# Kernel optimization log

Hardware: AMD Instinct MI355X
Metric: run time of the kernel (lower is better)

Reference implementation:

```python
import jax, jax.numpy as jnp
import numpy as np
from jax import lax

DIM = 128
EXP = 4
K = 7
B, D, H, W = 2, 48, 48, 48


def setup_inputs() -> dict:
    key = jax.random.key(0)
    ks = jax.random.split(key, 8)
    C, Ch = DIM, EXP * DIM
    x = jax.random.normal(ks[0], (B, C, D, H, W), dtype=jnp.float32)
    dw_w = jax.random.normal(ks[1], (C, 1, K, K, K), dtype=jnp.float32) * 0.05
    dw_b = jnp.zeros((C,), dtype=jnp.float32)
    ln_g = jnp.ones((C,), dtype=jnp.float32)
    ln_b = jnp.zeros((C,), dtype=jnp.float32)
    w1 = jax.random.normal(ks[2], (C, Ch), dtype=jnp.float32) * (1.0 / np.sqrt(C))
    b1 = jnp.zeros((Ch,), dtype=jnp.float32)
    grn_g = jnp.zeros((Ch,), dtype=jnp.float32)
    grn_b = jnp.zeros((Ch,), dtype=jnp.float32)
    w2 = jax.random.normal(ks[3], (Ch, C), dtype=jnp.float32) * (1.0 / np.sqrt(Ch))
    b2 = jnp.zeros((C,), dtype=jnp.float32)
    return {"x": x, "dw_w": dw_w, "dw_b": dw_b, "ln_g": ln_g, "ln_b": ln_b,
            "w1": w1, "b1": b1, "grn_g": grn_g, "grn_b": grn_b, "w2": w2, "b2": b2}


def reference(x, dw_w, dw_b, ln_g, ln_b, w1, b1, grn_g, grn_b, w2, b2):
    C = x.shape[1]
    pad = (K - 1) // 2
    # depthwise 3D conv, NCDHW
    y = lax.conv_general_dilated(
        x, dw_w, window_strides=(1, 1, 1),
        padding=[(pad, pad)] * 3,
        feature_group_count=C,
        dimension_numbers=("NCDHW", "OIDHW", "NCDHW"))
    y = y + dw_b[None, :, None, None, None]
    y = jnp.transpose(y, (0, 2, 3, 4, 1))  # [B,D,H,W,C] channels-last
    # LayerNorm over channels (eps=1e-6)
    mu = jnp.mean(y, axis=-1, keepdims=True)
    var = jnp.mean((y - mu) ** 2, axis=-1, keepdims=True)
    y = (y - mu) / jnp.sqrt(var + 1e-6) * ln_g + ln_b
    # pwconv1 + GELU (exact)
    h = jax.nn.gelu(jnp.einsum("bdhwc,ce->bdhwe", y, w1) + b1, approximate=False)
    # GRN: global L2 over spatial dims per channel, divisive norm over channel mean
    gx = jnp.sqrt(jnp.sum(h * h, axis=(1, 2, 3), keepdims=True))  # [B,1,1,1,Ch]
    nx = gx / (jnp.mean(gx, axis=-1, keepdims=True) + 1e-6)
    h = grn_g * (h * nx) + grn_b + h
    # pwconv2
    y = jnp.einsum("bdhwe,ec->bdhwc", h, w2) + b2
    y = jnp.transpose(y, (0, 4, 1, 2, 3))  # back to NCDHW
    return x + y
```

## Files before the change

### kernel.cpp

```cpp
#include <hip/hip_runtime.h>
#include <math.h>

#define PVOX 110592
#define CDIM 128
#define EDIM 512

typedef __attribute__((ext_vector_type(8))) short short8_t;
typedef __attribute__((ext_vector_type(4))) float float4_t;

__device__ __forceinline__ unsigned short f2bf(float f) {
  unsigned int u = __float_as_uint(f);
  unsigned int r = (u + 0x7FFFu + ((u >> 16) & 1u)) >> 16;
  return (unsigned short)r;
}
__device__ __forceinline__ float bf2f(unsigned short s) {
  return __uint_as_float(((unsigned int)s) << 16);
}
__device__ __forceinline__ int swz(int row, int col) {
  return (row << 7) + ((((col >> 3) ^ (row & 15)) << 3) | (col & 7));
}
__device__ __forceinline__ int swzO(int c, int p) {
  return (c << 7) + (p ^ ((c & 15) << 2));
}

__global__ __launch_bounds__(256) void k0_wprep(
    const float* __restrict__ w1, const float* __restrict__ w2,
    unsigned short* __restrict__ w1t, unsigned short* __restrict__ w2t) {
  int idx = blockIdx.x * 256 + threadIdx.x;
  int e = idx >> 7, c = idx & 127;
  w1t[e * 128 + c] = f2bf(w1[c * 512 + e]);
  w2t[c * 512 + e] = f2bf(w2[e * 128 + c]);
}

__global__ __launch_bounds__(576, 4) void k1_dwconv(
    const float* __restrict__ x, const float* __restrict__ dw_w,
    const float* __restrict__ dw_b, float* __restrict__ yconv) {
  __shared__ float sx[2][54 * 60];
  int bx = blockIdx.x;
  int dh = bx & 1;
  int c = (bx >> 1) & 127;
  int b = bx >> 8;
  int d0 = dh * 24;
  const float* xp = x + (size_t)(b * 128 + c) * PVOX;
  float* yp = yconv + (size_t)(b * 128 + c) * PVOX;
  const float* wbase = dw_w + c * 343;
  float bias = dw_b[c];
  int t = threadIdx.x;
  int h = t / 12, wc = t % 12;
  int w0 = wc * 4;
  for (int i = t; i < 2 * 54 * 60; i += 576) ((float*)sx)[i] = 0.f;
  __syncthreads();
  {
    int p = d0 - 3;
    if (p >= 0) {
      float4_t v = *(const float4_t*)&xp[((size_t)p * 48 + h) * 48 + w0];
      *(float4_t*)&sx[0][(h + 3) * 60 + 4 + w0] = v;
    }
  }
  float acc[7][4];
#pragma unroll
  for (int j = 0; j < 7; j++)
#pragma unroll
    for (int i = 0; i < 4; i++) acc[j][i] = bias;
  __syncthreads();

  for (int q = 0; q < 30; ++q) {
    int p = d0 - 3 + q;
    int pn = p + 1;
    bool ldok = (pn >= 0) && (pn <= 47) && (pn <= d0 + 26);
    float4_t stg = {0.f, 0.f, 0.f, 0.f};
    if (ldok) stg = *(const float4_t*)&xp[((size_t)pn * 48 + h) * 48 + w0];

    const float* bufr = sx[q & 1];
    if (p >= 0 && p <= 47) {
#pragma unroll
      for (int kh = 0; kh < 7; kh++) {
        const float* rp = &bufr[(h + kh) * 60 + w0];
        float4_t v0 = *(const float4_t*)&rp[0];
        float4_t v1 = *(const float4_t*)&rp[4];
        float4_t v2 = *(const float4_t*)&rp[8];
        float v[12] = {v0[0], v0[1], v0[2], v0[3], v1[0], v1[1], v1[2], v1[3],
                       v2[0], v2[1], v2[2], v2[3]};
#pragma unroll
        for (int kd = 0; kd < 7; kd++) {
          if ((unsigned)(q - kd) < 24u) {
            const float* wr = wbase + kd * 49 + kh * 7;
#pragma unroll
            for (int kw = 0; kw < 7; kw++) {
              float wv = wr[kw];
#pragma unroll
              for (int wi = 0; wi < 4; wi++)
                acc[6 - kd][wi] += wv * v[wi + kw + 1];
            }
          }
        }
      }
    }
    if (q >= 6) {
      int d = d0 + q - 6;
      float4_t o;
      o[0] = acc[0][0]; o[1] = acc[0][1]; o[2] = acc[0][2]; o[3] = acc[0][3];
      *(float4_t*)&yp[((size_t)d * 48 + h) * 48 + w0] = o;
    }
#pragma unroll
    for (int j = 0; j < 6; j++)
#pragma unroll
      for (int i = 0; i < 4; i++) acc[j][i] = acc[j + 1][i];
#pragma unroll
    for (int i = 0; i < 4; i++) acc[6][i] = bias;
    float* bufw = (float*)sx[(q + 1) & 1];
    *(float4_t*)&bufw[(h + 3) * 60 + 4 + w0] = stg;
    __syncthreads();
  }
}

__global__ __launch_bounds__(256) void k2_ln(
    const float* __restrict__ yconv, const float* __restrict__ ln_g,
    const float* __restrict__ ln_b, unsigned short* __restrict__ ycl) {
  __shared__ float sy[128 * 65];
  __shared__ float smean[64], srstd[64];
  int bx = blockIdx.x;
  int b = bx / 1728;
  int p0 = (bx % 1728) * 64;
  int t = threadIdx.x;
  int v = t & 63, c4 = t >> 6;
  const float* yp = yconv + (size_t)b * 128 * PVOX + p0;
  for (int cc = 0; cc < 32; cc++) {
    int c = cc * 4 + c4;
    sy[c * 65 + v] = yp[(size_t)c * PVOX + v];
  }
  __syncthreads();
  if (t < 64) {
    float s = 0.f, ss = 0.f;
    for (int c = 0; c < 128; c++) { float val = sy[c * 65 + t]; s += val; ss += val * val; }
    float mu = s * (1.f / 128.f);
    float var = ss * (1.f / 128.f) - mu * mu;
    smean[t] = mu; srstd[t] = rsqrtf(var + 1e-6f);
  }
  __syncthreads();
  unsigned short* op = ycl + ((size_t)b * PVOX + p0) * 128;
  for (int it = 0; it < 32; it++) {
    int idx = it * 256 + t;
    int vv = idx >> 7, c = idx & 127;
    float val = (sy[c * 65 + vv] - smean[vv]) * srstd[vv] * ln_g[c] + ln_b[c];
    op[vv * 128 + c] = f2bf(val);
  }
}

__global__ __launch_bounds__(256) void k3_pw1(
    const unsigned short* __restrict__ ycl, const unsigned short* __restrict__ w1t,
    const float* __restrict__ b1, unsigned short* __restrict__ h,
    float* __restrict__ gsum) {
  __shared__ short smem[2 * 128 * 128];
  short* sA = smem;
  short* sB = smem + 128 * 128;
  int bx = blockIdx.x;
  int et = bx & 3; int pt = bx >> 2;
  int e0 = et << 7;
  int b = (pt >= 864) ? 1 : 0;
  int t = threadIdx.x;
  for (int it = 0; it < 8; it++) {
    int flat = it * 2048 + t * 8;
    int row = flat >> 7, col = flat & 127;
    *(uint4*)&sA[swz(row, col)] = *(const uint4*)&ycl[((size_t)(pt * 128 + row)) * 128 + col];
    *(uint4*)&sB[swz(row, col)] = *(const uint4*)&w1t[(e0 + row) * 128 + col];
  }
  __syncthreads();
  int wave = t >> 6, lane = t & 63;
  int wm = (wave >> 1) * 64, wn = (wave & 1) * 64;
  int ln15 = lane & 15, q = lane >> 4;
  float4_t acc[4][4] = {};
  for (int kk = 0; kk < 4; kk++) {
    int k0 = kk * 32 + q * 8;
    short8_t af[4], bf[4];
#pragma unroll
    for (int i = 0; i < 4; i++)
      af[i] = *(const short8_t*)&sA[swz(wm + i * 16 + ln15, k0)];
#pragma unroll
    for (int j = 0; j < 4; j++)
      bf[j] = *(const short8_t*)&sB[swz(wn + j * 16 + ln15, k0)];
#pragma unroll
    for (int i = 0; i < 4; i++)
#pragma unroll
      for (int j = 0; j < 4; j++)
        acc[i][j] = __builtin_amdgcn_mfma_f32_16x16x32_bf16(af[i], bf[j], acc[i][j], 0, 0, 0);
  }
  __syncthreads();
  float biasv[4];
#pragma unroll
  for (int j = 0; j < 4; j++) biasv[j] = b1[e0 + wn + j * 16 + ln15];
  float ssq[4] = {0.f, 0.f, 0.f, 0.f};
#pragma unroll
  for (int i = 0; i < 4; i++) {
#pragma unroll
    for (int j = 0; j < 4; j++) {
      int e_local = wn + j * 16 + ln15;
#pragma unroll
      for (int r = 0; r < 4; r++) {
        float val = acc[i][j][r] + biasv[j];
        float g = 0.5f * val * (1.0f + erff(val * 0.70710678118f));
        ssq[j] += g * g;
        sA[swz(wm + i * 16 + q * 4 + r, e_local)] = (short)f2bf(g);
      }
    }
  }
#pragma unroll
  for (int j = 0; j < 4; j++) {
    ssq[j] += __shfl_xor(ssq[j], 16);
    ssq[j] += __shfl_xor(ssq[j], 32);
  }
  if (q == 0) {
#pragma unroll
    for (int j = 0; j < 4; j++)
      atomicAdd(&gsum[b * 512 + e0 + wn + j * 16 + ln15], ssq[j]);
  }
  __syncthreads();
  for (int it = 0; it < 8; it++) {
    int flat = it * 2048 + t * 8;
    int row = flat >> 7, col = flat & 127;
    *(uint4*)&h[((size_t)(pt * 128 + row)) * 512 + e0 + col] = *(const uint4*)&sA[swz(row, col)];
  }
}

__global__ __launch_bounds__(512) void k4_grn(
    const float* __restrict__ gsum, const float* __restrict__ grn_g,
    const float* __restrict__ grn_b, const float* __restrict__ w2,
    const float* __restrict__ b2, float* __restrict__ s, float* __restrict__ badd) {
  __shared__ float red[512];
  int t = threadIdx.x;
  for (int b = 0; b < 2; b++) {
    float gx = sqrtf(gsum[b * 512 + t]);
    red[t] = gx;
    __syncthreads();
    for (int off = 256; off > 0; off >>= 1) {
      if (t < off) red[t] += red[t + off];
      __syncthreads();
    }
    float mean = red[0] * (1.f / 512.f);
    __syncthreads();
    s[b * 512 + t] = 1.0f + grn_g[t] * (gx / (mean + 1e-6f));
  }
  if (t < 128) {
    float acc = b2[t];
    for (int e = 0; e < 512; e++) acc += grn_b[e] * w2[e * 128 + t];
    badd[t] = acc;
  }
}

__global__ __launch_bounds__(256) void k5_pw2(
    const unsigned short* __restrict__ h, const unsigned short* __restrict__ w2t,
    const float* __restrict__ s, const float* __restrict__ badd,
    const float* __restrict__ x, float* __restrict__ out) {
  __shared__ short smem[2 * 128 * 128];
  short* sA = smem;
  short* sB = smem + 128 * 128;
  int bx = blockIdx.x;
  int b = bx / 864;
  int p0 = (bx % 864) * 128;
  int vp0 = bx * 128;
  int t = threadIdx.x;
  int wave = t >> 6, lane = t & 63;
  int wm = (wave >> 1) * 64, wn = (wave & 1) * 64;
  int ln15 = lane & 15, q = lane >> 4;
  const float* sb = s + b * 512;
  float4_t acc[4][4] = {};
  for (int ec = 0; ec < 4; ec++) {
    int e0 = ec * 128;
    for (int it = 0; it < 8; it++) {
      int flat = it * 2048 + t * 8;
      int row = flat >> 7, col = flat & 127;
      uint4 raw = *(const uint4*)&h[((size_t)(vp0 + row)) * 512 + e0 + col];
      const unsigned short* us = (const unsigned short*)&raw;
      unsigned short ov[8];
#pragma unroll
      for (int i2 = 0; i2 < 8; i2++)
        ov[i2] = f2bf(bf2f(us[i2]) * sb[e0 + col + i2]);
      *(uint4*)&sA[swz(row, col)] = *(const uint4*)ov;
      *(uint4*)&sB[swz(row, col)] = *(const uint4*)&w2t[row * 512 + e0 + col];
    }
    __syncthreads();
    for (int kk = 0; kk < 4; kk++) {
      int k0 = kk * 32 + q * 8;
      short8_t af[4], bf[4];
#pragma unroll
      for (int i = 0; i < 4; i++)
        af[i] = *(const short8_t*)&sA[swz(wm + i * 16 + ln15, k0)];
#pragma unroll
      for (int j = 0; j < 4; j++)
        bf[j] = *(const short8_t*)&sB[swz(wn + j * 16 + ln15, k0)];
#pragma unroll
      for (int i = 0; i < 4; i++)
#pragma unroll
        for (int j = 0; j < 4; j++)
          acc[i][j] = __builtin_amdgcn_mfma_f32_16x16x32_bf16(af[i], bf[j], acc[i][j], 0, 0, 0);
    }
    __syncthreads();
  }
  float* sO = (float*)smem;
#pragma unroll
  for (int i = 0; i < 4; i++)
#pragma unroll
    for (int j = 0; j < 4; j++) {
      int c = wn + j * 16 + ln15;
#pragma unroll
      for (int r = 0; r < 4; r++)
        sO[swzO(c, wm + i * 16 + q * 4 + r)] = acc[i][j][r];
    }
  __syncthreads();
  for (int it = 0; it < 16; it++) {
    int flat4 = it * 256 + t;
    int c = flat4 >> 5, col4 = (flat4 & 31) * 4;
    float4_t v = *(const float4_t*)&sO[swzO(c, col4)];
    float bd = badd[c];
    size_t gi = (size_t)(b * 128 + c) * PVOX + p0 + col4;
    float4_t xv = *(const float4_t*)&x[gi];
    v[0] += bd + xv[0]; v[1] += bd + xv[1]; v[2] += bd + xv[2]; v[3] += bd + xv[3];
    *(float4_t*)&out[gi] = v;
  }
}

extern "C" void kernel_launch(void* const* d_in, const int* in_sizes, int n_in,
                              void* d_out, int out_size, void* d_ws, size_t ws_size,
                              hipStream_t stream) {
  (void)in_sizes; (void)n_in; (void)out_size; (void)ws_size;
  const float* x    = (const float*)d_in[0];
  const float* dw_w = (const float*)d_in[1];
  const float* dw_b = (const float*)d_in[2];
  const float* ln_g = (const float*)d_in[3];
  const float* ln_b = (const float*)d_in[4];
  const float* w1   = (const float*)d_in[5];
  const float* b1   = (const float*)d_in[6];
  const float* grn_g= (const float*)d_in[7];
  const float* grn_b= (const float*)d_in[8];
  const float* w2   = (const float*)d_in[9];
  const float* b2   = (const float*)d_in[10];
  float* outp = (float*)d_out;

  char* w = (char*)d_ws;
  float*          yconv = (float*)(w);
  unsigned short* ycl   = (unsigned short*)(w + 113246208);
  unsigned short* h     = (unsigned short*)(w + 169869312);
  float*          gsum  = (float*)(w + 396361728);
  float*          s     = (float*)(w + 396365824);
  float*          badd  = (float*)(w + 396369920);
  unsigned short* w1t   = (unsigned short*)(w + 396370432);
  unsigned short* w2t   = (unsigned short*)(w + 396501504);

  hipMemsetAsync(gsum, 0, 2 * 512 * sizeof(float), stream);
  k0_wprep<<<256, 256, 0, stream>>>(w1, w2, w1t, w2t);
  k1_dwconv<<<512, 576, 0, stream>>>(x, dw_w, dw_b, yconv);
  k2_ln<<<3456, 256, 0, stream>>>(yconv, ln_g, ln_b, ycl);
  k3_pw1<<<6912, 256, 0, stream>>>(ycl, w1t, b1, h, gsum);
  k4_grn<<<1, 512, 0, stream>>>(gsum, grn_g, grn_b, w2, b2, s, badd);
  k5_pw2<<<1728, 256, 0, stream>>>(h, w2t, s, badd, x, outp);
}
```

Before: 996.1 us.

## Retile depthwise conv into H/D tiles and loop pw1 over E tiles per block

```diff
diff --git a/kernel.cpp b/kernel.cpp
--- a/kernel.cpp
+++ b/kernel.cpp
@@ -32,29 +32,70 @@
   w2t[c * 512 + e] = f2bf(w2[e * 128 + c]);
 }
 
-__global__ __launch_bounds__(576, 4) void k1_dwconv(
+template <bool GUARD>
+__device__ __forceinline__ void conv_plane12(
+    const float* __restrict__ bufr, const float* __restrict__ wbase,
+    float (&acc)[7][4], int hl, int w0, int q) {
+#pragma unroll
+  for (int kh = 0; kh < 7; kh++) {
+    const float* rp = &bufr[(hl + kh) * 60 + w0];
+    float4_t v0 = *(const float4_t*)&rp[0];
+    float4_t v1 = *(const float4_t*)&rp[4];
+    float4_t v2 = *(const float4_t*)&rp[8];
+    float v[12] = {v0[0], v0[1], v0[2], v0[3], v1[0], v1[1], v1[2], v1[3],
+                   v2[0], v2[1], v2[2], v2[3]};
+#pragma unroll
+    for (int kd = 0; kd < 7; kd++) {
+      if (!GUARD || (unsigned)(q - kd) < 12u) {
+        const float* wr = wbase + kd * 49 + kh * 7;
+#pragma unroll
+        for (int kw = 0; kw < 7; kw++) {
+          float wv = wr[kw];
+#pragma unroll
+          for (int wi = 0; wi < 4; wi++)
+            acc[6 - kd][wi] += wv * v[wi + kw + 1];
+        }
+      }
+    }
+  }
+}
+
+__global__ __launch_bounds__(192) void k1_dwconv(
     const float* __restrict__ x, const float* __restrict__ dw_w,
     const float* __restrict__ dw_b, float* __restrict__ yconv) {
-  __shared__ float sx[2][54 * 60];
+  __shared__ float sx[2][22 * 60];
   int bx = blockIdx.x;
-  int dh = bx & 1;
-  int c = (bx >> 1) & 127;
-  int b = bx >> 8;
-  int d0 = dh * 24;
+  int h3 = bx % 3;
+  int dt4 = (bx / 3) & 3;
+  int c = (bx / 12) & 127;
+  int b = bx / 1536;
+  int dt0 = dt4 * 12, h0 = h3 * 16;
   const float* xp = x + (size_t)(b * 128 + c) * PVOX;
   float* yp = yconv + (size_t)(b * 128 + c) * PVOX;
   const float* wbase = dw_w + c * 343;
   float bias = dw_b[c];
   int t = threadIdx.x;
-  int h = t / 12, wc = t % 12;
-  int w0 = wc * 4;
-  for (int i = t; i < 2 * 54 * 60; i += 576) ((float*)sx)[i] = 0.f;
+  int hl = t / 12, wq = t % 12;
+  int w0 = wq * 4;
+  for (int i = t; i < 2 * 22 * 60; i += 192) ((float*)sx)[i] = 0.f;
   __syncthreads();
   {
-    int p = d0 - 3;
+    int p = dt0 - 3;
     if (p >= 0) {
-      float4_t v = *(const float4_t*)&xp[((size_t)p * 48 + h) * 48 + w0];
-      *(float4_t*)&sx[0][(h + 3) * 60 + 4 + w0] = v;
+      {
+        int gh = h0 - 3 + hl;
+        float4_t v = {0.f, 0.f, 0.f, 0.f};
+        if ((unsigned)gh < 48u)
+          v = *(const float4_t*)&xp[((size_t)p * 48 + gh) * 48 + wq * 4];
+        *(float4_t*)&sx[0][hl * 60 + 4 + wq * 4] = v;
+      }
+      if (t < 72) {
+        int gh = h0 + 13 + hl;
+        float4_t v = {0.f, 0.f, 0.f, 0.f};
+        if ((unsigned)gh < 48u)
+          v = *(const float4_t*)&xp[((size_t)p * 48 + gh) * 48 + wq * 4];
+        *(float4_t*)&sx[0][(hl + 16) * 60 + 4 + wq * 4] = v;
+      }
     }
   }
   float acc[7][4];
@@ -64,43 +105,54 @@
     for (int i = 0; i < 4; i++) acc[j][i] = bias;
   __syncthreads();
 
-  for (int q = 0; q < 30; ++q) {
-    int p = d0 - 3 + q;
-    int pn = p + 1;
-    bool ldok = (pn >= 0) && (pn <= 47) && (pn <= d0 + 26);
-    float4_t stg = {0.f, 0.f, 0.f, 0.f};
-    if (ldok) stg = *(const float4_t*)&xp[((size_t)pn * 48 + h) * 48 + w0];
-
-    const float* bufr = sx[q & 1];
-    if (p >= 0 && p <= 47) {
-#pragma unroll
-      for (int kh = 0; kh < 7; kh++) {
-        const float* rp = &bufr[(h + kh) * 60 + w0];
-        float4_t v0 = *(const float4_t*)&rp[0];
-        float4_t v1 = *(const float4_t*)&rp[4];
-        float4_t v2 = *(const float4_t*)&rp[8];
-        float v[12] = {v0[0], v0[1], v0[2], v0[3], v1[0], v1[1], v1[2], v1[3],
-                       v2[0], v2[1], v2[2], v2[3]};
-#pragma unroll
-        for (int kd = 0; kd < 7; kd++) {
-          if ((unsigned)(q - kd) < 24u) {
-            const float* wr = wbase + kd * 49 + kh * 7;
-#pragma unroll
-            for (int kw = 0; kw < 7; kw++) {
-              float wv = wr[kw];
-#pragma unroll
-              for (int wi = 0; wi < 4; wi++)
-                acc[6 - kd][wi] += wv * v[wi + kw + 1];
-            }
-          }
-        }
-      }
-    }
-    if (q >= 6) {
-      int d = d0 + q - 6;
+  for (int q = 0; q < 6; ++q) {
+    int p = dt0 - 3 + q, pn = p + 1;
+    bool ok = (pn >= 0);
+    float4_t sA = {0.f, 0.f, 0.f, 0.f}, sB = {0.f, 0.f, 0.f, 0.f};
+    if (ok) {
+      int gh = h0 - 3 + hl;
+      if ((unsigned)gh < 48u)
+        sA = *(const float4_t*)&xp[((size_t)pn * 48 + gh) * 48 + wq * 4];
+      if (t < 72) {
+        int gh2 = h0 + 13 + hl;
+        if ((unsigned)gh2 < 48u)
+          sB = *(const float4_t*)&xp[((size_t)pn * 48 + gh2) * 48 + wq * 4];
+      }
+    }
+    if (p >= 0)
+      conv_plane12<true>(sx[q & 1], wbase, acc, hl, w0, q);
+#pragma unroll
+    for (int j = 0; j < 6; j++)
+#pragma unroll
+      for (int i = 0; i < 4; i++) acc[j][i] = acc[j + 1][i];
+#pragma unroll
+    for (int i = 0; i < 4; i++) acc[6][i] = bias;
+    float* bw = (float*)sx[(q + 1) & 1];
+    *(float4_t*)&bw[hl * 60 + 4 + wq * 4] = sA;
+    if (t < 72) *(float4_t*)&bw[(hl + 16) * 60 + 4 + wq * 4] = sB;
+    __syncthreads();
+  }
+  for (int q = 6; q < 12; ++q) {
+    int pn = dt0 - 2 + q;
+    float4_t sA, sB = {0.f, 0.f, 0.f, 0.f};
+    {
+      int gh = h0 - 3 + hl;
+      float4_t v = {0.f, 0.f, 0.f, 0.f};
+      if ((unsigned)gh < 48u)
+        v = *(const float4_t*)&xp[((size_t)pn * 48 + gh) * 48 + wq * 4];
+      sA = v;
+      if (t < 72) {
+        int gh2 = h0 + 13 + hl;
+        if ((unsigned)gh2 < 48u)
+          sB = *(const float4_t*)&xp[((size_t)pn * 48 + gh2) * 48 + wq * 4];
+      }
+    }
+    conv_plane12<false>(sx[q & 1], wbase, acc, hl, w0, q);
+    {
+      int d = dt0 + q - 6;
       float4_t o;
       o[0] = acc[0][0]; o[1] = acc[0][1]; o[2] = acc[0][2]; o[3] = acc[0][3];
-      *(float4_t*)&yp[((size_t)d * 48 + h) * 48 + w0] = o;
+      *(float4_t*)&yp[((size_t)d * 48 + (h0 + hl)) * 48 + w0] = o;
     }
 #pragma unroll
     for (int j = 0; j < 6; j++)
@@ -108,8 +160,42 @@
       for (int i = 0; i < 4; i++) acc[j][i] = acc[j + 1][i];
 #pragma unroll
     for (int i = 0; i < 4; i++) acc[6][i] = bias;
-    float* bufw = (float*)sx[(q + 1) & 1];
-    *(float4_t*)&bufw[(h + 3) * 60 + 4 + w0] = stg;
+    float* bw = (float*)sx[(q + 1) & 1];
+    *(float4_t*)&bw[hl * 60 + 4 + wq * 4] = sA;
+    if (t < 72) *(float4_t*)&bw[(hl + 16) * 60 + 4 + wq * 4] = sB;
+    __syncthreads();
+  }
+  for (int q = 12; q < 18; ++q) {
+    int p = dt0 - 3 + q, pn = p + 1;
+    bool ok = (pn <= 47) && (pn <= dt0 + 14);
+    float4_t sA = {0.f, 0.f, 0.f, 0.f}, sB = {0.f, 0.f, 0.f, 0.f};
+    if (ok) {
+      int gh = h0 - 3 + hl;
+      if ((unsigned)gh < 48u)
+        sA = *(const float4_t*)&xp[((size_t)pn * 48 + gh) * 48 + wq * 4];
+      if (t < 72) {
+        int gh2 = h0 + 13 + hl;
+        if ((unsigned)gh2 < 48u)
+          sB = *(const float4_t*)&xp[((size_t)pn * 48 + gh2) * 48 + wq * 4];
+      }
+    }
+    if (p <= 47)
+      conv_plane12<true>(sx[q & 1], wbase, acc, hl, w0, q);
+    {
+      int d = dt0 + q - 6;
+      float4_t o;
+      o[0] = acc[0][0]; o[1] = acc[0][1]; o[2] = acc[0][2]; o[3] = acc[0][3];
+      *(float4_t*)&yp[((size_t)d * 48 + (h0 + hl)) * 48 + w0] = o;
+    }
+#pragma unroll
+    for (int j = 0; j < 6; j++)
+#pragma unroll
+      for (int i = 0; i < 4; i++) acc[j][i] = acc[j + 1][i];
+#pragma unroll
+    for (int i = 0; i < 4; i++) acc[6][i] = bias;
+    float* bw = (float*)sx[(q + 1) & 1];
+    *(float4_t*)&bw[hl * 60 + 4 + wq * 4] = sA;
+    if (t < 72) *(float4_t*)&bw[(hl + 16) * 60 + 4 + wq * 4] = sB;
     __syncthreads();
   }
 }
@@ -154,71 +240,77 @@
   __shared__ short smem[2 * 128 * 128];
   short* sA = smem;
   short* sB = smem + 128 * 128;
-  int bx = blockIdx.x;
-  int et = bx & 3; int pt = bx >> 2;
-  int e0 = et << 7;
+  int pt = blockIdx.x;
   int b = (pt >= 864) ? 1 : 0;
   int t = threadIdx.x;
   for (int it = 0; it < 8; it++) {
     int flat = it * 2048 + t * 8;
     int row = flat >> 7, col = flat & 127;
     *(uint4*)&sA[swz(row, col)] = *(const uint4*)&ycl[((size_t)(pt * 128 + row)) * 128 + col];
-    *(uint4*)&sB[swz(row, col)] = *(const uint4*)&w1t[(e0 + row) * 128 + col];
-  }
-  __syncthreads();
+  }
   int wave = t >> 6, lane = t & 63;
   int wm = (wave >> 1) * 64, wn = (wave & 1) * 64;
   int ln15 = lane & 15, q = lane >> 4;
-  float4_t acc[4][4] = {};
-  for (int kk = 0; kk < 4; kk++) {
-    int k0 = kk * 32 + q * 8;
-    short8_t af[4], bf[4];
-#pragma unroll
-    for (int i = 0; i < 4; i++)
-      af[i] = *(const short8_t*)&sA[swz(wm + i * 16 + ln15, k0)];
-#pragma unroll
-    for (int j = 0; j < 4; j++)
-      bf[j] = *(const short8_t*)&sB[swz(wn + j * 16 + ln15, k0)];
-#pragma unroll
-    for (int i = 0; i < 4; i++)
+  for (int et = 0; et < 4; et++) {
+    int e0 = et << 7;
+    for (int it = 0; it < 8; it++) {
+      int flat = it * 2048 + t * 8;
+      int row = flat >> 7, col = flat & 127;
+      *(uint4*)&sB[swz(row, col)] = *(const uint4*)&w1t[(e0 + row) * 128 + col];
+    }
+    __syncthreads();
+    float4_t acc[4][4] = {};
+    for (int kk = 0; kk < 4; kk++) {
+      int k0 = kk * 32 + q * 8;
+      short8_t af[4], bf[4];
+#pragma unroll
+      for (int i = 0; i < 4; i++)
+        af[i] = *(const short8_t*)&sA[swz(wm + i * 16 + ln15, k0)];
 #pragma unroll
       for (int j = 0; j < 4; j++)
-        acc[i][j] = __builtin_amdgcn_mfma_f32_16x16x32_bf16(af[i], bf[j], acc[i][j], 0, 0, 0);
-  }
-  __syncthreads();
-  float biasv[4];
-#pragma unroll
-  for (int j = 0; j < 4; j++) biasv[j] = b1[e0 + wn + j * 16 + ln15];
-  float ssq[4] = {0.f, 0.f, 0.f, 0.f};
-#pragma unroll
-  for (int i = 0; i < 4; i++) {
+        bf[j] = *(const short8_t*)&sB[swz(wn + j * 16 + ln15, k0)];
+#pragma unroll
+      for (int i = 0; i < 4; i++)
+#pragma unroll
+        for (int j = 0; j < 4; j++)
+          acc[i][j] = __builtin_amdgcn_mfma_f32_16x16x32_bf16(af[i], bf[j], acc[i][j], 0, 0, 0);
+    }
+    __syncthreads();
+    float biasv[4];
+#pragma unroll
+    for (int j = 0; j < 4; j++) biasv[j] = b1[e0 + wn + j * 16 + ln15];
+    float ssq[4] = {0.f, 0.f, 0.f, 0.f};
+#pragma unroll
+    for (int i = 0; i < 4; i++) {
+#pragma unroll
+      for (int j = 0; j < 4; j++) {
+        int e_local = wn + j * 16 + ln15;
+#pragma unroll
+        for (int r = 0; r < 4; r++) {
+          float val = acc[i][j][r] + biasv[j];
+          float g = 0.5f * val * (1.0f + erff(val * 0.70710678118f));
+          ssq[j] += g * g;
+          sB[swz(wm + i * 16 + q * 4 + r, e_local)] = (short)f2bf(g);
+        }
+      }
+    }
 #pragma unroll
     for (int j = 0; j < 4; j++) {
-      int e_local = wn + j * 16 + ln15;
-#pragma unroll
-      for (int r = 0; r < 4; r++) {
-        float val = acc[i][j][r] + biasv[j];
-        float g = 0.5f * val * (1.0f + erff(val * 0.70710678118f));
-        ssq[j] += g * g;
-        sA[swz(wm + i * 16 + q * 4 + r, e_local)] = (short)f2bf(g);
-      }
-    }
-  }
-#pragma unroll
-  for (int j = 0; j < 4; j++) {
-    ssq[j] += __shfl_xor(ssq[j], 16);
-    ssq[j] += __shfl_xor(ssq[j], 32);
-  }
-  if (q == 0) {
-#pragma unroll
-    for (int j = 0; j < 4; j++)
-      atomicAdd(&gsum[b * 512 + e0 + wn + j * 16 + ln15], ssq[j]);
-  }
-  __syncthreads();
-  for (int it = 0; it < 8; it++) {
-    int flat = it * 2048 + t * 8;
-    int row = flat >> 7, col = flat & 127;
-    *(uint4*)&h[((size_t)(pt * 128 + row)) * 512 + e0 + col] = *(const uint4*)&sA[swz(row, col)];
+      ssq[j] += __shfl_xor(ssq[j], 16);
+      ssq[j] += __shfl_xor(ssq[j], 32);
+    }
+    if (q == 0) {
+#pragma unroll
+      for (int j = 0; j < 4; j++)
+        atomicAdd(&gsum[b * 512 + e0 + wn + j * 16 + ln15], ssq[j]);
+    }
+    __syncthreads();
+    for (int it = 0; it < 8; it++) {
+      int flat = it * 2048 + t * 8;
+      int row = flat >> 7, col = flat & 127;
+      *(uint4*)&h[((size_t)(pt * 128 + row)) * 512 + e0 + col] = *(const uint4*)&sB[swz(row, col)];
+    }
+    __syncthreads();
   }
 }
 
@@ -348,9 +440,9 @@
 
   hipMemsetAsync(gsum, 0, 2 * 512 * sizeof(float), stream);
   k0_wprep<<<256, 256, 0, stream>>>(w1, w2, w1t, w2t);
-  k1_dwconv<<<512, 576, 0, stream>>>(x, dw_w, dw_b, yconv);
+  k1_dwconv<<<3072, 192, 0, stream>>>(x, dw_w, dw_b, yconv);
   k2_ln<<<3456, 256, 0, stream>>>(yconv, ln_g, ln_b, ycl);
-  k3_pw1<<<6912, 256, 0, stream>>>(ycl, w1t, b1, h, gsum);
+  k3_pw1<<<1728, 256, 0, stream>>>(ycl, w1t, b1, h, gsum);
   k4_grn<<<1, 512, 0, stream>>>(gsum, grn_g, grn_b, w2, b2, s, badd);
   k5_pw2<<<1728, 256, 0, stream>>>(h, w2t, s, badd, x, outp);
 }
```

Result: slower. 1.480 ms (+48.6%).
